# Kernel optimization log

Hardware: AMD Instinct MI355X
Metric: run time of the kernel (lower is better)

The kernel has to match this reference:

```python
import jax, jax.numpy as jnp
import numpy as np

N = 100000      # nodes
E = 1600000     # edges per node-kind graph
H = 2           # attention heads
F_IN = 64
F_OUT = 64
N_USER = 90000
D2 = 64
NB_CLASSES = 2


def setup_inputs() -> dict:
    key = jax.random.key(0)
    ks = jax.random.split(key, 16)
    xav = lambda k, shape: jax.random.normal(k, shape, jnp.float32) * np.sqrt(2.0 / (shape[-2] + shape[-1]))
    inp = {
        "h": jax.random.normal(ks[0], (N, F_IN), jnp.float32),
        "src0": jax.random.randint(ks[1], (E,), 0, N, jnp.int32),
        "trg0": jax.random.randint(ks[2], (E,), 0, N, jnp.int32),
        "src1": jax.random.randint(ks[3], (E,), 0, N, jnp.int32),
        "trg1": jax.random.randint(ks[4], (E,), 0, N, jnp.int32),
        # SpGATLayer params per node kind
        "w0": xav(ks[5], (H, F_IN, F_OUT)),
        "asrc0": xav(ks[6], (H, F_OUT)),   # attn_src squeezed from (H, F_OUT, 1)
        "atrg0": xav(ks[7], (H, F_OUT)),
        "w1": xav(ks[8], (H, F_IN, F_OUT)),
        "asrc1": xav(ks[9], (H, F_OUT)),
        "atrg1": xav(ks[10], (H, F_OUT)),
        # AdditiveAttention params (nn.Linear weights: [out, in])
        "aa_w1": xav(ks[11], (D2, F_IN)),
        "aa_w2": xav(ks[12], (D2, F_OUT)),
        "aa_m": xav(ks[13], (1, D2)),
        # final fc: in = d1 * (nb_node_kinds + 1) = 64 * 3
        "fc_w": xav(ks[14], (NB_CLASSES, F_OUT * 3)),
        "fc_b": jnp.zeros((NB_CLASSES,), jnp.float32),
        "n_user": N_USER,
    }
    return inp


def sp_gat_layer(h, w, a_src, a_trg, src, trg, n):
    # h: [N, F_IN]; w: [H, F_IN, F_OUT]
    hp = jnp.einsum("nf,hfo->hno", h, w)                  # [H, N, F_OUT]
    attn_src = jnp.einsum("hno,ho->nh", hp, a_src)        # [N, H]
    attn_trg = jnp.einsum("hno,ho->nh", hp, a_trg)        # [N, H]
    e = jax.nn.leaky_relu(attn_src[src] + attn_trg[trg], 0.2)  # [E, H]
    e = e - jnp.max(e)                                    # global max, as in source
    exp_e = jnp.exp(e)
    denom = jax.ops.segment_sum(exp_e, trg, num_segments=n)[trg] + 1e-16
    attn = (exp_e / denom)[:, :, None]                    # [E, H, 1]
    hp_nhf = jnp.transpose(hp, (1, 0, 2))                 # [N, H, F_OUT]
    h_weighted = hp_nhf[src] * attn                       # [E, H, F_OUT]
    out = jax.ops.segment_sum(h_weighted, trg, num_segments=n)  # [N, H, F_OUT]
    return out


def reference(h, src0, trg0, src1, trg1, w0, asrc0, atrg0, w1, asrc1, atrg1,
              aa_w1, aa_w2, aa_m, fc_w, fc_b, n_user):
    n = h.shape[0]
    # one SpGAT layer per node kind, then mean over heads (final-layer branch)
    x0 = sp_gat_layer(h, w0, asrc0, atrg0, src0, trg0, n).mean(axis=1)  # [N, F_OUT]
    x1 = sp_gat_layer(h, w1, asrc1, atrg1, src1, trg1, n).mean(axis=1)
    type_aware = jnp.stack([x0[:n_user], x1[:n_user]], axis=1)          # [n_user, 2, F_OUT]
    # AdditiveAttention
    feat = h[:n_user]                                                   # [n_user, F_IN]
    q = jnp.tanh(feat @ aa_w1.T[:, None, :].squeeze(1)[None][0] if False else
                 jnp.tanh(0.0))  # placeholder removed below
    q = jnp.tanh(feat[:, None, :] @ aa_w1.T + type_aware @ aa_w2.T)     # [n_user, 2, D2]
    scores = (q @ aa_m.T).squeeze(-1)                                   # [n_user, 2]
    beta = jax.nn.softmax(scores, axis=-1)
    type_fusion = jnp.einsum("nk,nkd->nd", beta, type_aware)[:, None, :]  # [n_user, 1, F_OUT]
    cat = jnp.concatenate([type_aware, type_fusion], axis=1).reshape(n_user, -1)  # [n_user, 3*F_OUT]
    logits = cat @ fc_w.T + fc_b
    return jax.nn.log_softmax(logits, axis=-1)
```

## Files before the change

### kernel.cpp

```cpp
#include <hip/hip_runtime.h>
#include <hip/hip_bf16.h>
#include <math.h>

#define N_NODES 100000
#define N_EDGES 1600000
#define N_USER  90000
#define NBUCK   256
#define BSZ     352
#define TILE    2048
#define TBLK    782
#define ACCB    22500
#define HPB     1024

typedef __attribute__((ext_vector_type(8))) short  short8;
typedef __attribute__((ext_vector_type(4))) float  floatx4;
typedef unsigned int  uint;
typedef unsigned short ushort;

__device__ __forceinline__ ushort f2bf(float x) {
  uint u = __float_as_uint(x);
  u += 0x7fffu + ((u >> 16) & 1u);
  return (ushort)(u >> 16);
}
__device__ __forceinline__ float bf2f(ushort v) { return __uint_as_float(((uint)v) << 16); }

__device__ __forceinline__ void split8(const float v[8], short8& hi, short8& lo) {
  #pragma unroll
  for (int j = 0; j < 8; ++j) {
    ushort h = f2bf(v[j]);
    hi[j] = (short)h;
    lo[j] = (short)f2bf(v[j] - bf2f(h));
  }
}
__device__ __forceinline__ void load_split8(const float* p, short8& hi, short8& lo) {
  const float4* q = (const float4*)p;
  float4 a = q[0], b = q[1];
  float v[8] = {a.x, a.y, a.z, a.w, b.x, b.y, b.z, b.w};
  split8(v, hi, lo);
}
__device__ __forceinline__ float fast_tanh(float x) {
  float t = __expf(2.f * x);
  return 1.f - 2.f / (t + 1.f);
}

__global__ __launch_bounds__(256) void stage1(
    const float* __restrict__ h,
    const float* __restrict__ wA,  const float* __restrict__ wB,
    const float* __restrict__ asA, const float* __restrict__ asB,
    const float* __restrict__ atA, const float* __restrict__ atB,
    uint* __restrict__ hpiA, uint* __restrict__ hpiB,
    float* __restrict__ attnsA, float* __restrict__ attnsB,
    float* __restrict__ attntA, float* __restrict__ attntB,
    const int* __restrict__ trgA, const int* __restrict__ trgB,
    int* __restrict__ bhist,
    int hpTot, int hpBase, int bhBase)
{
  __shared__ float part[4][16][4];
  __shared__ int hh[NBUCK];
  const int tid = threadIdx.x;

  if (blockIdx.x >= hpTot) {
    const int b2 = blockIdx.x - hpTot;
    const int layer = (b2 >= bhBase) ? 1 : 0;
    const int bid = b2 - layer * bhBase;
    const int* trg = layer ? trgB : trgA;
    int* bh = bhist + layer * NBUCK;
    hh[tid] = 0;
    __syncthreads();
    const int b0 = bid * TILE;
    #pragma unroll
    for (int j = 0; j < 8; ++j) {
      int e = b0 + j * 256 + tid;
      if (e < N_EDGES) {
        int t = trg[e];
        if (t < N_USER) atomicAdd(&hh[t / BSZ], 1);
      }
    }
    __syncthreads();
    if (hh[tid]) atomicAdd(&bh[tid], hh[tid]);
    return;
  }

  const int layer = (blockIdx.x >= hpBase) ? 1 : 0;
  const int bid = blockIdx.x - layer * hpBase;
  const float* w     = layer ? wB : wA;
  const float* a_src = layer ? asB : asA;
  const float* a_trg = layer ? atB : atA;
  uint*  hpi      = layer ? hpiB : hpiA;
  float* attn_src = layer ? attnsB : attnsA;
  float* attn_trg = layer ? attntB : attntA;

  const int lane = tid & 63, wv = tid >> 6;
  const int quad = lane >> 4, l15 = lane & 15;
  const int o = wv * 16 + l15;
  const float vas0 = a_src[o], vas1 = a_src[64 + o];
  const float vat0 = a_trg[o], vat1 = a_trg[64 + o];
  short8 b0h[2], b0l[2], b1h[2], b1l[2];
  #pragma unroll
  for (int ks = 0; ks < 2; ++ks) {
    float v0[8], v1[8];
    #pragma unroll
    for (int j = 0; j < 8; ++j) {
      int k = quad * 8 + j + ks * 32;
      v0[j] = w[k * 64 + o];
      v1[j] = w[4096 + k * 64 + o];
    }
    split8(v0, b0h[ks], b0l[ks]);
    split8(v1, b1h[ks], b1l[ks]);
  }
  for (int t = bid; t < N_NODES / 16; t += hpBase) {
    int m0 = t * 16, arow = m0 + l15;
    short8 ah[2], al[2];
    #pragma unroll
    for (int ks = 0; ks < 2; ++ks)
      load_split8(h + arow * 64 + quad * 8 + ks * 32, ah[ks], al[ks]);
    floatx4 c0 = {0.f, 0.f, 0.f, 0.f}, c1 = {0.f, 0.f, 0.f, 0.f};
    #pragma unroll
    for (int ks = 0; ks < 2; ++ks) {
      c0 = __builtin_amdgcn_mfma_f32_16x16x32_bf16(ah[ks], b0h[ks], c0, 0, 0, 0);
      c0 = __builtin_amdgcn_mfma_f32_16x16x32_bf16(ah[ks], b0l[ks], c0, 0, 0, 0);
      c0 = __builtin_amdgcn_mfma_f32_16x16x32_bf16(al[ks], b0h[ks], c0, 0, 0, 0);
      c1 = __builtin_amdgcn_mfma_f32_16x16x32_bf16(ah[ks], b1h[ks], c1, 0, 0, 0);
      c1 = __builtin_amdgcn_mfma_f32_16x16x32_bf16(ah[ks], b1l[ks], c1, 0, 0, 0);
      c1 = __builtin_amdgcn_mfma_f32_16x16x32_bf16(al[ks], b1h[ks], c1, 0, 0, 0);
    }
    #pragma unroll
    for (int r = 0; r < 4; ++r) {
      int n = m0 + quad * 4 + r;
      hpi[n * 64 + o] = (uint)f2bf(c0[r]) | ((uint)f2bf(c1[r]) << 16);
    }
    #pragma unroll
    for (int r = 0; r < 4; ++r) {
      float pas0 = c0[r] * vas0, pas1 = c1[r] * vas1;
      float pat0 = c0[r] * vat0, pat1 = c1[r] * vat1;
      #pragma unroll
      for (int m = 1; m < 16; m <<= 1) {
        pas0 += __shfl_xor(pas0, m, 64); pas1 += __shfl_xor(pas1, m, 64);
        pat0 += __shfl_xor(pat0, m, 64); pat1 += __shfl_xor(pat1, m, 64);
      }
      if (l15 == 0) {
        part[wv][quad * 4 + r][0] = pas0; part[wv][quad * 4 + r][1] = pas1;
        part[wv][quad * 4 + r][2] = pat0; part[wv][quad * 4 + r][3] = pat1;
      }
    }
    __syncthreads();
    if (tid < 64) {
      int row = tid & 15, which = tid >> 4;
      float v = part[0][row][which] + part[1][row][which]
              + part[2][row][which] + part[3][row][which];
      int n = m0 + row;
      if (which == 0)      attn_src[n * 2]     = v;
      else if (which == 1) attn_src[n * 2 + 1] = v;
      else if (which == 2) attn_trg[n * 2]     = v;
      else                 attn_trg[n * 2 + 1] = v;
    }
    __syncthreads();
  }
}

__global__ __launch_bounds__(256) void scanb2(const int* __restrict__ bhist,
                                              int* __restrict__ bstart, int* __restrict__ bcur)
{
  const int layer = blockIdx.x;
  const int* bh = bhist + layer * NBUCK;
  int* bs = bstart + layer * (NBUCK + 1);
  int* bc = bcur + layer * NBUCK * 16;
  __shared__ int s[256];
  int v = bh[threadIdx.x];
  s[threadIdx.x] = v;
  __syncthreads();
  for (int d = 1; d < 256; d <<= 1) {
    int t = (threadIdx.x >= d) ? s[threadIdx.x - d] : 0;
    __syncthreads();
    s[threadIdx.x] += t;
    __syncthreads();
  }
  int excl = s[threadIdx.x] - v;
  bs[threadIdx.x] = excl;
  bc[threadIdx.x * 16] = excl;
  if (threadIdx.x == 255) bs[256] = s[255];
}

__global__ __launch_bounds__(256) void bucket2(
    const int* __restrict__ srcA, const int* __restrict__ srcB,
    const int* __restrict__ trgA, const int* __restrict__ trgB,
    int* __restrict__ bcur, uint2* __restrict__ pairbufA, uint2* __restrict__ pairbufB, int base)
{
  const int layer = (blockIdx.x >= base) ? 1 : 0;
  const int bid = blockIdx.x - layer * base;
  const int* src = layer ? srcB : srcA;
  const int* trg = layer ? trgB : trgA;
  int* bc = bcur + layer * NBUCK * 16;
  uint2* pairbuf = layer ? pairbufB : pairbufA;

  __shared__ uint2 plds[TILE];
  __shared__ int bcnt[NBUCK], bscan[NBUCK], gbase[NBUCK];
  const int tid = threadIdx.x;
  const int b0 = bid * TILE;
  bcnt[tid] = 0;
  __syncthreads();
  int myb[8], myr[8];
  uint2 myp[8];
  #pragma unroll
  for (int j = 0; j < 8; ++j) {
    int e = b0 + j * 256 + tid;
    myb[j] = -1;
    if (e < N_EDGES) {
      int t = trg[e];
      if (t < N_USER) {
        int b = t / BSZ;
        myb[j] = b;
        myr[j] = atomicAdd(&bcnt[b], 1);
        myp[j].x = (uint)src[e];
        myp[j].y = (uint)t;
      }
    }
  }
  __syncthreads();
  gbase[tid] = atomicAdd(&bc[tid * 16], bcnt[tid]);
  bscan[tid] = bcnt[tid];
  __syncthreads();
  for (int d = 1; d < 256; d <<= 1) {
    int v = (tid >= d) ? bscan[tid - d] : 0;
    __syncthreads();
    bscan[tid] += v;
    __syncthreads();
  }
  #pragma unroll
  for (int j = 0; j < 8; ++j)
    if (myb[j] >= 0) plds[bscan[myb[j]] - bcnt[myb[j]] + myr[j]] = myp[j];
  __syncthreads();
  int total = bscan[NBUCK - 1];
  for (int i = tid; i < total; i += 256) {
    uint2 pr = plds[i];
    int b = (int)pr.y / BSZ;
    int idx = gbase[b] + (i - (bscan[b] - bcnt[b]));
    if (idx >= 0 && idx < N_EDGES) pairbuf[idx] = pr;
  }
}

__global__ __launch_bounds__(256) void fine2(
    const uint2* __restrict__ pairbufA, const uint2* __restrict__ pairbufB,
    const int* __restrict__ bstart,
    int* __restrict__ offsA, int* __restrict__ offsB,
    int* __restrict__ csrA,  int* __restrict__ csrB,
    const float* __restrict__ attnsA, const float* __restrict__ attnsB,
    const float* __restrict__ attntA, const float* __restrict__ attntB,
    float2* __restrict__ wgtA, float2* __restrict__ wgtB, int base)
{
  const int layer = (blockIdx.x >= base) ? 1 : 0;
  const int b = blockIdx.x - layer * base;
  const uint2* pairbuf = layer ? pairbufB : pairbufA;
  const int* bs = bstart + layer * (NBUCK + 1);
  int* offs = layer ? offsB : offsA;
  int* csr_src = layer ? csrB : csrA;
  const float* attn_src = layer ? attnsB : attnsA;
  const float* attn_trg = layer ? attntB : attntA;
  float2* wgt = layer ? wgtB : wgtA;

  __shared__ int cnt[BSZ + 1];
  __shared__ int cur[BSZ];
  const int tid = threadIdx.x;
  const int t0 = b * BSZ;
  const int nt = min(BSZ, N_USER - t0);
  const int pbeg = bs[b], pend = bs[b + 1];
  for (int j = tid; j <= BSZ; j += 256) cnt[j] = 0;
  __syncthreads();
  for (int i = pbeg + tid; i < pend; i += 256) {
    int tl = (int)pairbuf[i].y - t0;
    tl = min(max(tl, 0), BSZ - 1);
    atomicAdd(&cnt[tl], 1);
  }
  __syncthreads();
  if (tid == 0) {
    int run = 0;
    for (int j = 0; j < nt; ++j) { int c = cnt[j]; cnt[j] = run; run += c; }
    cnt[nt] = run;
  }
  __syncthreads();
  for (int j = tid; j < nt; j += 256) {
    offs[t0 + j] = pbeg + cnt[j];
    cur[j] = cnt[j];
  }
  if (tid == 0 && t0 + nt == N_USER) offs[N_USER] = pbeg + cnt[nt];
  __syncthreads();
  const float2* as2 = (const float2*)attn_src;
  const float2* at2 = (const float2*)attn_trg;
  for (int i = pbeg + tid; i < pend; i += 256) {
    uint2 pr = pairbuf[i];
    int s = min((int)pr.x, N_NODES - 1);
    int tt = min((int)pr.y, N_USER - 1);
    int tl = min(max(tt - t0, 0), BSZ - 1);
    float2 as = as2[s];
    float2 at = at2[tt];
    float e0 = as.x + at.x; e0 = (e0 > 0.f) ? e0 : 0.2f * e0;
    float e1 = as.y + at.y; e1 = (e1 > 0.f) ? e1 : 0.2f * e1;
    int p = pbeg + atomicAdd(&cur[tl], 1);
    p = min(max(p, 0), N_EDGES - 1);
    csr_src[p] = s;
    wgt[p] = make_float2(__expf(e0), __expf(e1));
  }
}

__global__ __launch_bounds__(256) void accum2(
    const int* __restrict__ offsA, const int* __restrict__ offsB,
    const int* __restrict__ csrA,  const int* __restrict__ csrB,
    const float2* __restrict__ wgtA, const float2* __restrict__ wgtB,
    const uint* __restrict__ hpiA, const uint* __restrict__ hpiB,
    float* __restrict__ xA, float* __restrict__ xB, int base)
{
  const int layer = (blockIdx.x >= base) ? 1 : 0;
  const int bid = blockIdx.x - layer * base;
  const int* offs = layer ? offsB : offsA;
  const int* csr_src = layer ? csrB : csrA;
  const float2* wgt = layer ? wgtB : wgtA;
  const uint* hpi = layer ? hpiB : hpiA;
  float* x = layer ? xB : xA;

  const int lane = threadIdx.x & 63, wv = threadIdx.x >> 6;
  int n = bid * 4 + wv;
  if (n >= N_USER) return;
  int beg = max(0, offs[n]);
  int end = min(offs[n + 1], N_EDGES);
  beg = __builtin_amdgcn_readfirstlane(beg);
  end = __builtin_amdgcn_readfirstlane(end);
  int deg = end - beg;
  float acc0 = 0.f, acc1 = 0.f, den0 = 0.f, den1 = 0.f;
  for (int base2 = 0; base2 < deg; base2 += 64) {
    int rem = min(64, deg - base2);
    int sv = csr_src[beg + base2 + min(lane, rem - 1)];
    sv = min(max(sv, 0), N_NODES - 1);
    int nfull = rem & ~7;
    for (int j = 0; j < nfull; j += 8) {
      int ss[8]; uint pv[8]; float2 W[8];
      #pragma unroll
      for (int u = 0; u < 8; ++u) ss[u] = __builtin_amdgcn_readlane(sv, j + u);
      #pragma unroll
      for (int u = 0; u < 8; ++u) pv[u] = (hpi + (size_t)ss[u] * 64)[lane];
      #pragma unroll
      for (int u = 0; u < 8; ++u) W[u] = wgt[beg + base2 + j + u];
      #pragma unroll
      for (int u = 0; u < 8; ++u) {
        den0 += W[u].x; den1 += W[u].y;
        acc0 += W[u].x * bf2f((ushort)(pv[u] & 0xffffu));
        acc1 += W[u].y * bf2f((ushort)(pv[u] >> 16));
      }
    }
    if (nfull < rem) {
      int j = nfull;
      int ss[8]; uint pv[8]; float2 W[8];
      #pragma unroll
      for (int u = 0; u < 8; ++u) ss[u] = __builtin_amdgcn_readlane(sv, min(j + u, rem - 1));
      #pragma unroll
      for (int u = 0; u < 8; ++u) pv[u] = (hpi + (size_t)ss[u] * 64)[lane];
      #pragma unroll
      for (int u = 0; u < 8; ++u)
        W[u] = (j + u < rem) ? wgt[beg + base2 + j + u] : make_float2(0.f, 0.f);
      #pragma unroll
      for (int u = 0; u < 8; ++u) {
        den0 += W[u].x; den1 += W[u].y;
        acc0 += W[u].x * bf2f((ushort)(pv[u] & 0xffffu));
        acc1 += W[u].y * bf2f((ushort)(pv[u] >> 16));
      }
    }
  }
  x[n * 64 + lane] = 0.5f * (acc0 / (den0 + 1e-16f) + acc1 / (den1 + 1e-16f));
}

__global__ __launch_bounds__(256) void final_mfma(
    const float* __restrict__ h, const float* __restrict__ x0, const float* __restrict__ x1,
    const float* __restrict__ aa_w1, const float* __restrict__ aa_w2, const float* __restrict__ aa_m,
    const float* __restrict__ fc_w, const float* __restrict__ fc_b, float* __restrict__ out)
{
  __shared__ float aam_s[64], fcw_s[384], fcb_s[2];
  __shared__ float scw0[4][16], scw1[4][16];
  const int tid = threadIdx.x;
  if (tid < 64)  aam_s[tid] = aa_m[tid];
  for (int i = tid; i < 384; i += 256) fcw_s[i] = fc_w[i];
  if (tid < 2)   fcb_s[tid] = fc_b[tid];
  const int lane = tid & 63, wv = tid >> 6, quad = lane >> 4, l15 = lane & 15;
  const int d = wv * 16 + l15;
  short8 b1h[2], b1l[2], b2h[2], b2l[2];
  #pragma unroll
  for (int ks = 0; ks < 2; ++ks) {
    load_split8(aa_w1 + d * 64 + quad * 8 + ks * 32, b1h[ks], b1l[ks]);
    load_split8(aa_w2 + d * 64 + quad * 8 + ks * 32, b2h[ks], b2l[ks]);
  }
  __syncthreads();
  for (int t = blockIdx.x; t < N_USER / 16; t += gridDim.x) {
    int m0 = t * 16, arow = m0 + l15;
    const int erow = m0 + wv * 4 + quad;
    float4 ev0 = *(const float4*)(x0 + erow * 64 + l15 * 4);
    float4 ev1 = *(const float4*)(x1 + erow * 64 + l15 * 4);
    short8 ahh[2], ahl[2], a0h[2], a0l[2], a1h[2], a1l[2];
    #pragma unroll
    for (int ks = 0; ks < 2; ++ks) {
      load_split8(h  + arow * 64 + quad * 8 + ks * 32, ahh[ks], ahl[ks]);
      load_split8(x0 + arow * 64 + quad * 8 + ks * 32, a0h[ks], a0l[ks]);
      load_split8(x1 + arow * 64 + quad * 8 + ks * 32, a1h[ks], a1l[ks]);
    }
    floatx4 t1a = {0.f,0.f,0.f,0.f}, t20a = {0.f,0.f,0.f,0.f}, t21a = {0.f,0.f,0.f,0.f};
    #pragma unroll
    for (int ks = 0; ks < 2; ++ks) {
      t1a  = __builtin_amdgcn_mfma_f32_16x16x32_bf16(ahh[ks], b1h[ks], t1a, 0, 0, 0);
      t1a  = __builtin_amdgcn_mfma_f32_16x16x32_bf16(ahh[ks], b1l[ks], t1a, 0, 0, 0);
      t1a  = __builtin_amdgcn_mfma_f32_16x16x32_bf16(ahl[ks], b1h[ks], t1a, 0, 0, 0);
      t20a = __builtin_amdgcn_mfma_f32_16x16x32_bf16(a0h[ks], b2h[ks], t20a, 0, 0, 0);
      t20a = __builtin_amdgcn_mfma_f32_16x16x32_bf16(a0h[ks], b2l[ks], t20a, 0, 0, 0);
      t20a = __builtin_amdgcn_mfma_f32_16x16x32_bf16(a0l[ks], b2h[ks], t20a, 0, 0, 0);
      t21a = __builtin_amdgcn_mfma_f32_16x16x32_bf16(a1h[ks], b2h[ks], t21a, 0, 0, 0);
      t21a = __builtin_amdgcn_mfma_f32_16x16x32_bf16(a1h[ks], b2l[ks], t21a, 0, 0, 0);
      t21a = __builtin_amdgcn_mfma_f32_16x16x32_bf16(a1l[ks], b2h[ks], t21a, 0, 0, 0);
    }
    float am = aam_s[d];
    #pragma unroll
    for (int r = 0; r < 4; ++r) {
      float q0 = fast_tanh(t1a[r] + t20a[r]);
      float q1 = fast_tanh(t1a[r] + t21a[r]);
      float p0 = q0 * am, p1 = q1 * am;
      #pragma unroll
      for (int m = 1; m < 16; m <<= 1) { p0 += __shfl_xor(p0, m, 64); p1 += __shfl_xor(p1, m, 64); }
      if (l15 == 0) { scw0[wv][quad * 4 + r] = p0; scw1[wv][quad * 4 + r] = p1; }
    }
    __syncthreads();
    {
      int row = wv * 4 + quad, n = m0 + row;
      float s0 = scw0[0][row] + scw0[1][row] + scw0[2][row] + scw0[3][row];
      float s1 = scw1[0][row] + scw1[1][row] + scw1[2][row] + scw1[3][row];
      float mx = fmaxf(s0, s1);
      float e0 = __expf(s0 - mx), e1 = __expf(s1 - mx);
      float inv = 1.f / (e0 + e1);
      float b0 = e0 * inv, b1 = e1 * inv;
      float a0[4] = {ev0.x, ev0.y, ev0.z, ev0.w};
      float a1[4] = {ev1.x, ev1.y, ev1.z, ev1.w};
      float pc0 = 0.f, pc1 = 0.f;
      #pragma unroll
      for (int c = 0; c < 4; ++c) {
        int o = l15 * 4 + c;
        float fv = b0 * a0[c] + b1 * a1[c];
        pc0 += fcw_s[o] * a0[c] + fcw_s[64 + o] * a1[c] + fcw_s[128 + o] * fv;
        pc1 += fcw_s[192 + o] * a0[c] + fcw_s[256 + o] * a1[c] + fcw_s[320 + o] * fv;
      }
      #pragma unroll
      for (int m = 1; m < 16; m <<= 1) { pc0 += __shfl_xor(pc0, m, 64); pc1 += __shfl_xor(pc1, m, 64); }
      if (l15 == 0) {
        float l0 = pc0 + fcb_s[0], l1 = pc1 + fcb_s[1];
        float lm = fmaxf(l0, l1);
        float lse = lm + logf(__expf(l0 - lm) + __expf(l1 - lm));
        out[n * 2] = l0 - lse;
        out[n * 2 + 1] = l1 - lse;
      }
    }
    __syncthreads();
  }
}

extern "C" void kernel_launch(void* const* d_in, const int* in_sizes, int n_in,
                              void* d_out, int out_size, void* d_ws, size_t ws_size,
                              hipStream_t stream)
{
  const float* h     = (const float*)d_in[0];
  const int*   src0  = (const int*)d_in[1];
  const int*   trg0  = (const int*)d_in[2];
  const int*   src1  = (const int*)d_in[3];
  const int*   trg1  = (const int*)d_in[4];
  const float* w0    = (const float*)d_in[5];
  const float* asrc0 = (const float*)d_in[6];
  const float* atrg0 = (const float*)d_in[7];
  const float* w1    = (const float*)d_in[8];
  const float* asrc1 = (const float*)d_in[9];
  const float* atrg1 = (const float*)d_in[10];
  const float* aa_w1 = (const float*)d_in[11];
  const float* aa_w2 = (const float*)d_in[12];
  const float* aa_m  = (const float*)d_in[13];
  const float* fc_w  = (const float*)d_in[14];
  const float* fc_b  = (const float*)d_in[15];
  float* out = (float*)d_out;

  const int nl = (ws_size >= (size_t)172 * 1024 * 1024) ? 2 : 1;
  const size_t L = (size_t)(nl - 1);

  char* ws = (char*)d_ws;
  size_t off = 0;
  auto alloc = [&](size_t bytes) -> void* {
    void* p = ws + off;
    off = (off + bytes + 255) & ~(size_t)255;
    return p;
  };
  uint*   hpi      = (uint*)alloc((size_t)nl * N_NODES * 64 * 4);
  float*  attn_src = (float*)alloc((size_t)nl * N_NODES * 2 * 4);
  float*  attn_trg = (float*)alloc((size_t)nl * N_NODES * 2 * 4);
  float*  x0       = (float*)alloc((size_t)N_USER * 64 * 4);
  float*  x1       = (float*)alloc((size_t)N_USER * 64 * 4);
  int*    offs     = (int*)alloc((size_t)nl * (N_USER + 1) * 4);
  int*    csr      = (int*)alloc((size_t)nl * N_EDGES * 4);
  uint2*  pairbuf  = (uint2*)alloc((size_t)nl * N_EDGES * 8);
  float2* wgt      = (float2*)alloc((size_t)nl * N_EDGES * 8);
  int*    bhist    = (int*)alloc((size_t)2 * NBUCK * 4);
  int*    bstart   = (int*)alloc((size_t)2 * (NBUCK + 1) * 4);
  int*    bcur     = (int*)alloc((size_t)2 * NBUCK * 16 * 4);

  uint*   hpi1     = hpi + L * (size_t)N_NODES * 64;
  float*  attns1   = attn_src + L * (size_t)N_NODES * 2;
  float*  attnt1   = attn_trg + L * (size_t)N_NODES * 2;
  int*    offs1    = offs + L * (size_t)(N_USER + 1);
  int*    csr1     = csr + L * (size_t)N_EDGES;
  uint2*  pairbuf1 = pairbuf + L * (size_t)N_EDGES;
  float2* wgt1     = wgt + L * (size_t)N_EDGES;

  if (nl == 2) {
    hipMemsetAsync(bhist, 0, (size_t)2 * NBUCK * 4, stream);
    hipLaunchKernelGGL(stage1, dim3(2 * HPB + 2 * TBLK), dim3(256), 0, stream,
                       h, w0, w1, asrc0, asrc1, atrg0, atrg1,
                       hpi, hpi1, attn_src, attns1, attn_trg, attnt1,
                       trg0, trg1, bhist, 2 * HPB, HPB, TBLK);
    hipLaunchKernelGGL(scanb2, dim3(2), dim3(256), 0, stream, bhist, bstart, bcur);
    hipLaunchKernelGGL(bucket2, dim3(2 * TBLK), dim3(256), 0, stream,
                       src0, src1, trg0, trg1, bcur, pairbuf, pairbuf1, TBLK);
    hipLaunchKernelGGL(fine2, dim3(2 * NBUCK), dim3(256), 0, stream,
                       pairbuf, pairbuf1, bstart, offs, offs1, csr, csr1,
                       attn_src, attns1, attn_trg, attnt1, wgt, wgt1, NBUCK);
    hipLaunchKernelGGL(accum2, dim3(2 * ACCB), dim3(256), 0, stream,
                       offs, offs1, csr, csr1, wgt, wgt1, hpi, hpi1, x0, x1, ACCB);
  } else {
    for (int layer = 0; layer < 2; ++layer) {
      const float* w    = layer ? w1 : w0;
      const float* asrc = layer ? asrc1 : asrc0;
      const float* atrg = layer ? atrg1 : atrg0;
      const int*   src  = layer ? src1 : src0;
      const int*   trg  = layer ? trg1 : trg0;
      float*       x    = layer ? x1 : x0;
      hipMemsetAsync(bhist, 0, (size_t)NBUCK * 4, stream);
      hipLaunchKernelGGL(stage1, dim3(HPB + TBLK), dim3(256), 0, stream,
                         h, w, w, asrc, asrc, atrg, atrg,
                         hpi, hpi, attn_src, attn_src, attn_trg, attn_trg,
                         trg, trg, bhist, HPB, HPB, TBLK);
      hipLaunchKernelGGL(scanb2, dim3(1), dim3(256), 0, stream, bhist, bstart, bcur);
      hipLaunchKernelGGL(bucket2, dim3(TBLK), dim3(256), 0, stream,
                         src, src, trg, trg, bcur, pairbuf, pairbuf, TBLK);
      hipLaunchKernelGGL(fine2, dim3(NBUCK), dim3(256), 0, stream,
                         pairbuf, pairbuf, bstart, offs, offs, csr, csr,
                         attn_src, attn_src, attn_trg, attn_trg, wgt, wgt, NBUCK);
      hipLaunchKernelGGL(accum2, dim3(ACCB), dim3(256), 0, stream,
                         offs, offs, csr, csr, wgt, wgt, hpi, hpi, x, x, ACCB);
    }
  }
  hipLaunchKernelGGL(final_mfma, dim3(1875), dim3(256), 0, stream,
                     h, x0, x1, aa_w1, aa_w2, aa_m, fc_w, fc_b, out);
}
```

Before: 447.8 us.

## Pack edge pairs into 32-bit words and swizzle accumulate blocks per XCD

The bucketing pass now stores each edge as a single 32-bit word, holding the source id in the low 17 bits and the target's offset within its bucket in the high bits, instead of an 8-byte pair. This halves the pair buffer's write and read traffic and shrinks the workspace threshold for the two-layer path. Separately, the accumulate kernel remaps block indices so that each group of XCDs handles one layer, which should keep each layer's hp features and CSR data local to fewer L2 caches. The remapping assumes round-robin dispatch of blocks across 8 XCDs, and the packing relies on node ids fitting in 17 bits.

```diff
diff --git a/kernel.cpp b/kernel.cpp
--- a/kernel.cpp
+++ b/kernel.cpp
@@ -184,14 +184,14 @@
 __global__ __launch_bounds__(256) void bucket2(
     const int* __restrict__ srcA, const int* __restrict__ srcB,
     const int* __restrict__ trgA, const int* __restrict__ trgB,
-    int* __restrict__ bcur, uint2* __restrict__ pairbufA, uint2* __restrict__ pairbufB, int base)
+    int* __restrict__ bcur, uint* __restrict__ pairbufA, uint* __restrict__ pairbufB, int base)
 {
   const int layer = (blockIdx.x >= base) ? 1 : 0;
   const int bid = blockIdx.x - layer * base;
   const int* src = layer ? srcB : srcA;
   const int* trg = layer ? trgB : trgA;
   int* bc = bcur + layer * NBUCK * 16;
-  uint2* pairbuf = layer ? pairbufB : pairbufA;
+  uint* pairbuf = layer ? pairbufB : pairbufA;
 
   __shared__ uint2 plds[TILE];
   __shared__ int bcnt[NBUCK], bscan[NBUCK], gbase[NBUCK];
@@ -200,7 +200,7 @@
   bcnt[tid] = 0;
   __syncthreads();
   int myb[8], myr[8];
-  uint2 myp[8];
+  uint myp[8];
   #pragma unroll
   for (int j = 0; j < 8; ++j) {
     int e = b0 + j * 256 + tid;
@@ -209,10 +209,10 @@
       int t = trg[e];
       if (t < N_USER) {
         int b = t / BSZ;
+        int tl = t - b * BSZ;
         myb[j] = b;
         myr[j] = atomicAdd(&bcnt[b], 1);
-        myp[j].x = (uint)src[e];
-        myp[j].y = (uint)t;
+        myp[j] = (uint)src[e] | ((uint)tl << 17);
       }
     }
   }
@@ -228,19 +228,19 @@
   }
   #pragma unroll
   for (int j = 0; j < 8; ++j)
-    if (myb[j] >= 0) plds[bscan[myb[j]] - bcnt[myb[j]] + myr[j]] = myp[j];
+    if (myb[j] >= 0) plds[bscan[myb[j]] - bcnt[myb[j]] + myr[j]] = make_uint2(myp[j], (uint)myb[j]);
   __syncthreads();
   int total = bscan[NBUCK - 1];
   for (int i = tid; i < total; i += 256) {
     uint2 pr = plds[i];
-    int b = (int)pr.y / BSZ;
+    int b = (int)pr.y;
     int idx = gbase[b] + (i - (bscan[b] - bcnt[b]));
-    if (idx >= 0 && idx < N_EDGES) pairbuf[idx] = pr;
+    if (idx >= 0 && idx < N_EDGES) pairbuf[idx] = pr.x;
   }
 }
 
 __global__ __launch_bounds__(256) void fine2(
-    const uint2* __restrict__ pairbufA, const uint2* __restrict__ pairbufB,
+    const uint* __restrict__ pairbufA, const uint* __restrict__ pairbufB,
     const int* __restrict__ bstart,
     int* __restrict__ offsA, int* __restrict__ offsB,
     int* __restrict__ csrA,  int* __restrict__ csrB,
@@ -250,7 +250,7 @@
 {
   const int layer = (blockIdx.x >= base) ? 1 : 0;
   const int b = blockIdx.x - layer * base;
-  const uint2* pairbuf = layer ? pairbufB : pairbufA;
+  const uint* pairbuf = layer ? pairbufB : pairbufA;
   const int* bs = bstart + layer * (NBUCK + 1);
   int* offs = layer ? offsB : offsA;
   int* csr_src = layer ? csrB : csrA;
@@ -267,8 +267,7 @@
   for (int j = tid; j <= BSZ; j += 256) cnt[j] = 0;
   __syncthreads();
   for (int i = pbeg + tid; i < pend; i += 256) {
-    int tl = (int)pairbuf[i].y - t0;
-    tl = min(max(tl, 0), BSZ - 1);
+    int tl = min((int)(pairbuf[i] >> 17), BSZ - 1);
     atomicAdd(&cnt[tl], 1);
   }
   __syncthreads();
@@ -287,10 +286,10 @@
   const float2* as2 = (const float2*)attn_src;
   const float2* at2 = (const float2*)attn_trg;
   for (int i = pbeg + tid; i < pend; i += 256) {
-    uint2 pr = pairbuf[i];
-    int s = min((int)pr.x, N_NODES - 1);
-    int tt = min((int)pr.y, N_USER - 1);
-    int tl = min(max(tt - t0, 0), BSZ - 1);
+    uint v = pairbuf[i];
+    int s = min((int)(v & 0x1FFFFu), N_NODES - 1);
+    int tl = min((int)(v >> 17), BSZ - 1);
+    int tt = min(t0 + tl, N_USER - 1);
     float2 as = as2[s];
     float2 at = at2[tt];
     float e0 = as.x + at.x; e0 = (e0 > 0.f) ? e0 : 0.2f * e0;
@@ -307,10 +306,17 @@
     const int* __restrict__ csrA,  const int* __restrict__ csrB,
     const float2* __restrict__ wgtA, const float2* __restrict__ wgtB,
     const uint* __restrict__ hpiA, const uint* __restrict__ hpiB,
-    float* __restrict__ xA, float* __restrict__ xB, int base)
-{
-  const int layer = (blockIdx.x >= base) ? 1 : 0;
-  const int bid = blockIdx.x - layer * base;
+    float* __restrict__ xA, float* __restrict__ xB, int base, int swz)
+{
+  int layer, bid;
+  if (swz) {
+    const int xcd = blockIdx.x & 7, idx = blockIdx.x >> 3;
+    layer = xcd >> 2;
+    bid = idx * 4 + (xcd & 3);
+  } else {
+    layer = (blockIdx.x >= base) ? 1 : 0;
+    bid = blockIdx.x - layer * base;
+  }
   const int* offs = layer ? offsB : offsA;
   const int* csr_src = layer ? csrB : csrA;
   const float2* wgt = layer ? wgtB : wgtA;
@@ -477,7 +483,7 @@
   const float* fc_b  = (const float*)d_in[15];
   float* out = (float*)d_out;
 
-  const int nl = (ws_size >= (size_t)172 * 1024 * 1024) ? 2 : 1;
+  const int nl = (ws_size >= (size_t)162 * 1024 * 1024) ? 2 : 1;
   const size_t L = (size_t)(nl - 1);
 
   char* ws = (char*)d_ws;
@@ -494,7 +500,7 @@
   float*  x1       = (float*)alloc((size_t)N_USER * 64 * 4);
   int*    offs     = (int*)alloc((size_t)nl * (N_USER + 1) * 4);
   int*    csr      = (int*)alloc((size_t)nl * N_EDGES * 4);
-  uint2*  pairbuf  = (uint2*)alloc((size_t)nl * N_EDGES * 8);
+  uint*   pairbuf  = (uint*)alloc((size_t)nl * N_EDGES * 4);
   float2* wgt      = (float2*)alloc((size_t)nl * N_EDGES * 8);
   int*    bhist    = (int*)alloc((size_t)2 * NBUCK * 4);
   int*    bstart   = (int*)alloc((size_t)2 * (NBUCK + 1) * 4);
@@ -505,7 +511,7 @@
   float*  attnt1   = attn_trg + L * (size_t)N_NODES * 2;
   int*    offs1    = offs + L * (size_t)(N_USER + 1);
   int*    csr1     = csr + L * (size_t)N_EDGES;
-  uint2*  pairbuf1 = pairbuf + L * (size_t)N_EDGES;
+  uint*   pairbuf1 = pairbuf + L * (size_t)N_EDGES;
   float2* wgt1     = wgt + L * (size_t)N_EDGES;
 
   if (nl == 2) {
@@ -521,7 +527,7 @@
                        pairbuf, pairbuf1, bstart, offs, offs1, csr, csr1,
                        attn_src, attns1, attn_trg, attnt1, wgt, wgt1, NBUCK);
     hipLaunchKernelGGL(accum2, dim3(2 * ACCB), dim3(256), 0, stream,
-                       offs, offs1, csr, csr1, wgt, wgt1, hpi, hpi1, x0, x1, ACCB);
+                       offs, offs1, csr, csr1, wgt, wgt1, hpi, hpi1, x0, x1, ACCB, 1);
   } else {
     for (int layer = 0; layer < 2; ++layer) {
       const float* w    = layer ? w1 : w0;
@@ -542,7 +548,7 @@
                          pairbuf, pairbuf, bstart, offs, offs, csr, csr,
                          attn_src, attn_src, attn_trg, attn_trg, wgt, wgt, NBUCK);
       hipLaunchKernelGGL(accum2, dim3(ACCB), dim3(256), 0, stream,
-                         offs, offs, csr, csr, wgt, wgt, hpi, hpi, x, x, ACCB);
+                         offs, offs, csr, csr, wgt, wgt, hpi, hpi, x, x, ACCB, 0);
     }
   }
   hipLaunchKernelGGL(final_mfma, dim3(1875), dim3(256), 0, stream,
```

After: 444.0 us. Within noise of the previous version (-0.8%).
